# Optimization experiments

Measured on AMD Instinct MI355X. Metric: run time of the kernel, lower is better.

The kernel has to match this reference:

```python
import jax, jax.numpy as jnp
import numpy as np

EPS = 1e-5
NUM_HEADS = 8


def bn(x, gamma, beta, mean, var):
    # eval-mode BatchNorm2d over channel dim (NCHW)
    inv = gamma / jnp.sqrt(var + EPS)
    return x * inv[None, :, None, None] + (beta - mean * inv)[None, :, None, None]


def conv1x1(x, w):
    # w: (O, I, 1, 1) -> pointwise matmul
    return jnp.einsum('bchw,oc->bohw', x, w[:, :, 0, 0])


def conv3x3(x, w):
    return jax.lax.conv_general_dilated(
        x, w, window_strides=(1, 1), padding=((1, 1), (1, 1)),
        dimension_numbers=('NCHW', 'OIHW', 'NCHW'))


def setup_inputs() -> dict:
    key = jax.random.key(0)
    ks = jax.random.split(key, 4)
    B, C, H, W = 2, 256, 64, 64
    return {
        'x': jax.random.normal(ks[0], (B, C, H, W), jnp.float32),
        'w_qkv': jax.random.normal(ks[1], (3 * C, C, 1, 1), jnp.float32) * 0.05,
        'w_local': jax.random.normal(ks[2], (C, C, 3, 3), jnp.float32) * 0.05,
        'local_gamma': jnp.ones((C,), jnp.float32),
        'local_beta': jnp.zeros((C,), jnp.float32),
        'local_mean': jnp.zeros((C,), jnp.float32),
        'local_var': jnp.ones((C,), jnp.float32),
        'w_proj': jax.random.normal(ks[3], (C, C, 1, 1), jnp.float32) * 0.05,
        'proj_gamma': jnp.ones((C,), jnp.float32),
        'proj_beta': jnp.zeros((C,), jnp.float32),
        'proj_mean': jnp.zeros((C,), jnp.float32),
        'proj_var': jnp.ones((C,), jnp.float32),
    }


def reference(x, w_qkv, w_local, local_gamma, local_beta, local_mean, local_var,
              w_proj, proj_gamma, proj_beta, proj_mean, proj_var):
    B, C, H, W = x.shape
    hd = C // NUM_HEADS
    scale = hd ** -0.5
    # qkv: (B, 3C, H, W) -> (B, 3, heads, hd, N)
    qkv = conv1x1(x, w_qkv).reshape(B, 3, NUM_HEADS, hd, H * W)
    q, k, v = qkv[:, 0], qkv[:, 1], qkv[:, 2]  # each (B, heads, hd, N)
    attn = jnp.einsum('bhdn,bhdm->bhnm', q, k) * scale  # (B, heads, N, N)
    attn = jax.nn.softmax(attn, axis=-1)
    out = jnp.einsum('bhnm,bhdm->bhdn', attn, v).reshape(B, C, H, W)
    local_out = bn(conv3x3(x, w_local), local_gamma, local_beta, local_mean, local_var)
    return bn(conv1x1(out + local_out, w_proj), proj_gamma, proj_beta, proj_mean, proj_var)
```

## Files before the change

### kernel.cpp

```cpp
#include <hip/hip_runtime.h>

#define EPSV 1e-5f

typedef unsigned short u16;
typedef unsigned int u32;
typedef __attribute__((ext_vector_type(8))) short bf16x8;
typedef __attribute__((ext_vector_type(4))) float f32x4;

__device__ __forceinline__ u16 f2bf(float f) {
  u32 u = __float_as_uint(f);
  u32 r = (u + 0x7FFFu + ((u >> 16) & 1u)) >> 16;
  return (u16)r;
}
__device__ __forceinline__ float fexp2(float x) {
  float r;
  asm("v_exp_f32 %0, %1" : "=v"(r) : "v"(x));
  return r;
}

#define MFMA(a, b, c) __builtin_amdgcn_mfma_f32_16x16x32_bf16((a), (b), (c), 0, 0, 0)

__global__ __launch_bounds__(256) void prep_kernel(
    const float* __restrict__ x, const float* __restrict__ wqkv,
    const float* __restrict__ wproj, const float* __restrict__ wloc,
    u16* __restrict__ xT, u16* __restrict__ wqkvb,
    u16* __restrict__ wprojb, u16* __restrict__ wb) {
  __shared__ float Ls[16][260];
  const int bid = blockIdx.x;
  const int tid = threadIdx.x;
  if (bid < 512) {
    const int nt = bid & 15, cb = (bid >> 4) & 15, b = bid >> 8;
    const int cc0 = tid >> 6, n4 = (tid & 63) * 4;
    const float* xb = x + ((size_t)(b * 256 + cb * 16)) * 4096 + nt * 256;
#pragma unroll
    for (int j = 0; j < 4; j++) {
      int cc = j * 4 + cc0;
      *(float4*)&Ls[cc][n4] = *(const float4*)(xb + (size_t)cc * 4096 + n4);
    }
    __syncthreads();
    const int n = tid;
    u16 buf[16];
#pragma unroll
    for (int c = 0; c < 16; c++) buf[c] = f2bf(Ls[c][n]);
    u16* dst = xT + ((size_t)cb * 8192 + b * 4096 + nt * 256 + n) * 16;
    *(uint4*)(dst) = *(uint4*)&buf[0];
    *(uint4*)(dst + 8) = *(uint4*)&buf[8];
  } else {
    const int r = bid - 512, c = tid;
    const float QSCALE = 0.17677669529663687f * 1.4426950408889634f;
    if (r < 768) {
      float sc = (r < 256) ? QSCALE : 1.0f;
      wqkvb[r * 256 + c] = f2bf(wqkv[r * 256 + c] * sc);
    } else if (r < 1024) {
      int o = r - 768;
      wprojb[o * 256 + c] = f2bf(wproj[o * 256 + c]);
    } else {
      int o = r - 1024;
      const float* src = wloc + ((size_t)o * 256 + c) * 9;
#pragma unroll
      for (int tap = 0; tap < 9; tap++)
        wb[tap * 65536 + o * 256 + c] = f2bf(src[tap]);
    }
  }
}

__global__ __launch_bounds__(256, 4) void qkvconv_kernel(
    const u16* __restrict__ xT, const u16* __restrict__ wqkvb,
    const u16* __restrict__ wb,
    const float* __restrict__ g, const float* __restrict__ be,
    const float* __restrict__ mu, const float* __restrict__ var,
    u16* __restrict__ Qg, u16* __restrict__ Kg, u16* __restrict__ Vtg,
    u16* __restrict__ localT) {
  const int bid = blockIdx.x;
  const int tid = threadIdx.x, lane = tid & 63, wv = tid >> 6;
  const int n16 = lane & 15, G = lane >> 4;
  if (bid < 768) {
    const int nB = (bid & 63) * 128;
    const int oB = (bid >> 6) * 64;
    const int waveO = oB + (wv >> 1) * 32;
    const int waveN = nB + (wv & 1) * 64;
    f32x4 acc[2][4] = {};
    const u16* Ap = wqkvb + (size_t)(waveO + n16) * 256 + G * 8;
    const u16* Bp = xT + ((size_t)(G >> 1) * 8192 + waveN + n16) * 16 + (G & 1) * 8;
    for (int c0 = 0; c0 < 256; c0 += 32) {
      bf16x8 a0 = *(const bf16x8*)(Ap + c0);
      bf16x8 a1 = *(const bf16x8*)(Ap + 16 * 256 + c0);
      const u16* bp = Bp + (size_t)(c0 >> 4) * 131072;
      bf16x8 b0 = *(const bf16x8*)(bp);
      bf16x8 b1 = *(const bf16x8*)(bp + 256);
      bf16x8 b2 = *(const bf16x8*)(bp + 512);
      bf16x8 b3 = *(const bf16x8*)(bp + 768);
      acc[0][0] = MFMA(a0, b0, acc[0][0]);
      acc[0][1] = MFMA(a0, b1, acc[0][1]);
      acc[0][2] = MFMA(a0, b2, acc[0][2]);
      acc[0][3] = MFMA(a0, b3, acc[0][3]);
      acc[1][0] = MFMA(a1, b0, acc[1][0]);
      acc[1][1] = MFMA(a1, b1, acc[1][1]);
      acc[1][2] = MFMA(a1, b2, acc[1][2]);
      acc[1][3] = MFMA(a1, b3, acc[1][3]);
    }
    const int which = oB >> 8;
    if (which < 2) {
      u16* base = which ? Kg : Qg;
#pragma unroll
      for (int i = 0; i < 2; i++) {
        int o0 = waveO + i * 16 + G * 4;
        int h = (o0 >> 5) & 7, d0 = o0 & 31;
#pragma unroll
        for (int j = 0; j < 4; j++) {
          int s = waveN + j * 16 + n16;
          int b = s >> 12, n = s & 4095;
          u16 pk[4];
#pragma unroll
          for (int r = 0; r < 4; r++) pk[r] = f2bf(acc[i][j][r]);
          *(uint2*)(base + ((size_t)(b * 8 + h) * 4096 + n) * 32 + d0) = *(uint2*)pk;
        }
      }
    } else {
#pragma unroll
      for (int i = 0; i < 2; i++) {
        int o0 = waveO + i * 16 + G * 4;
        int h = (o0 >> 5) & 7, d0 = o0 & 31;
#pragma unroll
        for (int j = 0; j < 4; j++) {
          int s = waveN + j * 16 + n16;
          int b = s >> 12, n = s & 4095;
          u16* vp = Vtg + ((size_t)(b * 8 + h) * 32 + d0) * 4096 + n;
#pragma unroll
          for (int r = 0; r < 4; r++) vp[(size_t)r * 4096] = f2bf(acc[i][j][r]);
        }
      }
    }
  } else {
    const int r0 = bid - 768;
    const int nB = (r0 & 127) * 64;
    const int oB = (r0 >> 7) * 64;
    const int waveO = oB + (wv >> 1) * 32;
    const int waveN = nB + (wv & 1) * 32;
    const int y = (nB >> 6) & 63;
    const int x0 = waveN & 63;
    f32x4 acc[2][2] = {};
    const u16* Ap = wb + (size_t)(waveO + n16) * 256 + G * 8;
    const u16* Bp = xT + ((size_t)(G >> 1) * 8192 + waveN + n16) * 16 + (G & 1) * 8;
    const bf16x8 z = {0, 0, 0, 0, 0, 0, 0, 0};
    for (int c0 = 0; c0 < 256; c0 += 32) {
      const u16* bp = Bp + (size_t)(c0 >> 4) * 131072;
      const u16* ap = Ap + c0;
#pragma unroll
      for (int tap = 0; tap < 9; tap++) {
        const int dy = tap / 3 - 1, dx = tap % 3 - 1;
        int yy = y + dy;
        if ((unsigned)yy >= 64u) continue;
        bf16x8 a0 = *(const bf16x8*)(ap + (size_t)tap * 65536);
        bf16x8 a1 = *(const bf16x8*)(ap + (size_t)tap * 65536 + 16 * 256);
        const int off = dy * 64 + dx;
        bf16x8 b0, b1;
        if (dx == 0) {
          b0 = *(const bf16x8*)(bp + (ptrdiff_t)off * 16);
          b1 = *(const bf16x8*)(bp + (ptrdiff_t)(off + 16) * 16);
        } else {
          bool v0 = (unsigned)(x0 + n16 + dx) < 64u;
          bool v1 = (unsigned)(x0 + 16 + n16 + dx) < 64u;
          int o0 = v0 ? off : 0;
          int o1 = v1 ? (off + 16) : 16;
          bf16x8 t0 = *(const bf16x8*)(bp + (ptrdiff_t)o0 * 16);
          bf16x8 t1 = *(const bf16x8*)(bp + (ptrdiff_t)o1 * 16);
          b0 = v0 ? t0 : z;
          b1 = v1 ? t1 : z;
        }
        acc[0][0] = MFMA(a0, b0, acc[0][0]);
        acc[0][1] = MFMA(a0, b1, acc[0][1]);
        acc[1][0] = MFMA(a1, b0, acc[1][0]);
        acc[1][1] = MFMA(a1, b1, acc[1][1]);
      }
    }
#pragma unroll
    for (int i = 0; i < 2; i++) {
      int o0 = waveO + i * 16 + G * 4;
      float inv[4], sh[4];
#pragma unroll
      for (int r = 0; r < 4; r++) {
        int o = o0 + r;
        float iv = g[o] * rsqrtf(var[o] + EPSV);
        inv[r] = iv; sh[r] = be[o] - mu[o] * iv;
      }
#pragma unroll
      for (int j = 0; j < 2; j++) {
        int s = waveN + j * 16 + n16;
        u16 pk[4];
#pragma unroll
        for (int r = 0; r < 4; r++) pk[r] = f2bf(acc[i][j][r] * inv[r] + sh[r]);
        *(uint2*)(localT + ((size_t)(o0 >> 4) * 8192 + s) * 16 + (o0 & 15)) = *(uint2*)pk;
      }
    }
  }
}

__global__ __launch_bounds__(256, 4) void flash_mfma_kernel(
    const u16* __restrict__ Qg, const u16* __restrict__ Kg,
    const u16* __restrict__ Vtg, u16* __restrict__ attnT) {
  __shared__ u32 Ps[4][32 * 36];
  __shared__ float MX[2][64][20];
  const int bid = blockIdx.x;
  const int bh = bid >> 6, qt = bid & 63;
  const int tid = threadIdx.x, lane = tid & 63, w = tid >> 6;
  const int n16 = lane & 15, G = lane >> 4;
  const int g = w >> 1, mh = w & 1;
  const int b = bh >> 3, h = bh & 7;
  const int qbase = qt * 64 + g * 32;

  const u16* Qp = Qg + ((size_t)bh * 4096 + qbase) * 32;
  const bf16x8 qf0 = *(const bf16x8*)(Qp + (size_t)n16 * 32 + G * 8);
  const bf16x8 qf1 = *(const bf16x8*)(Qp + (size_t)(16 + n16) * 32 + G * 8);

  f32x4 O00 = {0.f,0.f,0.f,0.f}, O01 = {0.f,0.f,0.f,0.f};
  f32x4 O10 = {0.f,0.f,0.f,0.f}, O11 = {0.f,0.f,0.f,0.f};
  float m0 = -3.0e38f, m1 = -3.0e38f, l0 = 0.f, l1 = 0.f;

  const u16* Kb = Kg + ((size_t)bh * 4096 + mh * 2048) * 32;
  const u16* Vb = Vtg + (size_t)bh * 32 * 4096 + mh * 2048;
  u32* Pw = Ps[w];

  bf16x8 kf0 = *(const bf16x8*)(Kb + (size_t)n16 * 32 + G * 8);
  bf16x8 kf1 = *(const bf16x8*)(Kb + (size_t)(16 + n16) * 32 + G * 8);
  bf16x8 kf2 = *(const bf16x8*)(Kb + (size_t)(32 + n16) * 32 + G * 8);
  bf16x8 kf3 = *(const bf16x8*)(Kb + (size_t)(48 + n16) * 32 + G * 8);

  for (int it = 0; it < 32; ++it) {
    const f32x4 z = {0.f, 0.f, 0.f, 0.f};
    f32x4 S0[4], S1[4];
    S0[0] = MFMA(kf0, qf0, z); S1[0] = MFMA(kf0, qf1, z);
    S0[1] = MFMA(kf1, qf0, z); S1[1] = MFMA(kf1, qf1, z);
    S0[2] = MFMA(kf2, qf0, z); S1[2] = MFMA(kf2, qf1, z);
    S0[3] = MFMA(kf3, qf0, z); S1[3] = MFMA(kf3, qf1, z);

    {
      const u16* Kn = Kb + (size_t)(((it + 1) & 31) * 64) * 32;
      kf0 = *(const bf16x8*)(Kn + (size_t)n16 * 32 + G * 8);
      kf1 = *(const bf16x8*)(Kn + (size_t)(16 + n16) * 32 + G * 8);
      kf2 = *(const bf16x8*)(Kn + (size_t)(32 + n16) * 32 + G * 8);
      kf3 = *(const bf16x8*)(Kn + (size_t)(48 + n16) * 32 + G * 8);
    }

    float mt0 = fmaxf(fmaxf(S0[0].x, S0[0].y), fmaxf(S0[0].z, S0[0].w));
    float mt1 = fmaxf(fmaxf(S1[0].x, S1[0].y), fmaxf(S1[0].z, S1[0].w));
#pragma unroll
    for (int t = 1; t < 4; t++) {
      mt0 = fmaxf(mt0, fmaxf(fmaxf(S0[t].x, S0[t].y), fmaxf(S0[t].z, S0[t].w)));
      mt1 = fmaxf(mt1, fmaxf(fmaxf(S1[t].x, S1[t].y), fmaxf(S1[t].z, S1[t].w)));
    }
    mt0 = fmaxf(mt0, __shfl_xor(mt0, 16, 64));
    mt0 = fmaxf(mt0, __shfl_xor(mt0, 32, 64));
    mt1 = fmaxf(mt1, __shfl_xor(mt1, 16, 64));
    mt1 = fmaxf(mt1, __shfl_xor(mt1, 32, 64));
    float mn0 = fmaxf(m0, mt0), mn1 = fmaxf(m1, mt1);
    if (__any((mt0 > m0) | (mt1 > m1))) {
      float a0 = fexp2(m0 - mn0);
      float a1 = fexp2(m1 - mn1);
      l0 *= a0; l1 *= a1;
      O00 *= a0; O01 *= a0; O10 *= a1; O11 *= a1;
    }
    m0 = mn0; m1 = mn1;

#pragma unroll
    for (int t = 0; t < 4; t++) {
      float p0 = fexp2(S0[t].x - m0), p1 = fexp2(S0[t].y - m0);
      float p2 = fexp2(S0[t].z - m0), p3 = fexp2(S0[t].w - m0);
      l0 += (p0 + p1) + (p2 + p3);
      uint2 pr;
      pr.x = __builtin_amdgcn_perm(__float_as_uint(p1), __float_as_uint(p0), 0x07060302u);
      pr.y = __builtin_amdgcn_perm(__float_as_uint(p3), __float_as_uint(p2), 0x07060302u);
      *(uint2*)&Pw[n16 * 36 + 8 * t + 2 * G] = pr;
      float q0 = fexp2(S1[t].x - m1), q1 = fexp2(S1[t].y - m1);
      float q2 = fexp2(S1[t].z - m1), q3 = fexp2(S1[t].w - m1);
      l1 += (q0 + q1) + (q2 + q3);
      uint2 qr;
      qr.x = __builtin_amdgcn_perm(__float_as_uint(q1), __float_as_uint(q0), 0x07060302u);
      qr.y = __builtin_amdgcn_perm(__float_as_uint(q3), __float_as_uint(q2), 0x07060302u);
      *(uint2*)&Pw[(16 + n16) * 36 + 8 * t + 2 * G] = qr;
    }

#pragma unroll
    for (int c = 0; c < 2; c++) {
      const u16* Vp = Vb + (size_t)it * 64 + c * 32 + G * 8;
      bf16x8 va0 = *(const bf16x8*)(Vp + (size_t)n16 * 4096);
      bf16x8 va1 = *(const bf16x8*)(Vp + (size_t)(16 + n16) * 4096);
      union { uint4 u; bf16x8 v; } B0, B1;
      B0.u = *(uint4*)&Pw[n16 * 36 + 16 * c + 4 * G];
      B1.u = *(uint4*)&Pw[(16 + n16) * 36 + 16 * c + 4 * G];
      O00 = MFMA(va0, B0.v, O00);
      O01 = MFMA(va1, B0.v, O01);
      O10 = MFMA(va0, B1.v, O10);
      O11 = MFMA(va1, B1.v, O11);
    }
  }

  if (mh == 1) {
    float* dst = &MX[g][lane][0];
    *(f32x4*)(dst + 0)  = O00;
    *(f32x4*)(dst + 4)  = O01;
    *(f32x4*)(dst + 8)  = O10;
    *(f32x4*)(dst + 12) = O11;
    dst[16] = m0; dst[17] = l0; dst[18] = m1; dst[19] = l1;
  }
  __syncthreads();
  if (mh == 0) {
    const float* src = &MX[g][lane][0];
    f32x4 P00 = *(const f32x4*)(src + 0);
    f32x4 P01 = *(const f32x4*)(src + 4);
    f32x4 P10 = *(const f32x4*)(src + 8);
    f32x4 P11 = *(const f32x4*)(src + 12);
    float pm0 = src[16], pl0 = src[17], pm1 = src[18], pl1 = src[19];

    float M0 = fmaxf(m0, pm0);
    float se0 = fexp2(m0 - M0), so0 = fexp2(pm0 - M0);
    float M1 = fmaxf(m1, pm1);
    float se1 = fexp2(m1 - M1), so1 = fexp2(pm1 - M1);
    float ls0 = l0 * se0 + pl0 * so0;
    float ls1 = l1 * se1 + pl1 * so1;
    ls0 += __shfl_xor(ls0, 16, 64);
    ls0 += __shfl_xor(ls0, 32, 64);
    ls1 += __shfl_xor(ls1, 16, 64);
    ls1 += __shfl_xor(ls1, 32, 64);
    const float rl0 = 1.0f / ls0, rl1 = 1.0f / ls1;

    const int s0 = b * 4096 + qbase + n16;
    const int s1 = s0 + 16;
    const int cb0 = h * 2, cb1 = h * 2 + 1;
    u16 pk[4];
#pragma unroll
    for (int r = 0; r < 4; r++) pk[r] = f2bf((O00[r] * se0 + P00[r] * so0) * rl0);
    *(uint2*)(attnT + ((size_t)cb0 * 8192 + s0) * 16 + G * 4) = *(uint2*)pk;
#pragma unroll
    for (int r = 0; r < 4; r++) pk[r] = f2bf((O01[r] * se0 + P01[r] * so0) * rl0);
    *(uint2*)(attnT + ((size_t)cb1 * 8192 + s0) * 16 + G * 4) = *(uint2*)pk;
#pragma unroll
    for (int r = 0; r < 4; r++) pk[r] = f2bf((O10[r] * se1 + P10[r] * so1) * rl1);
    *(uint2*)(attnT + ((size_t)cb0 * 8192 + s1) * 16 + G * 4) = *(uint2*)pk;
#pragma unroll
    for (int r = 0; r < 4; r++) pk[r] = f2bf((O11[r] * se1 + P11[r] * so1) * rl1);
    *(uint2*)(attnT + ((size_t)cb1 * 8192 + s1) * 16 + G * 4) = *(uint2*)pk;
  }
}

__global__ __launch_bounds__(256, 4) void proj_mfma_kernel(
    const u16* __restrict__ attnT, const u16* __restrict__ localT,
    const u16* __restrict__ wprojb,
    const float* __restrict__ g, const float* __restrict__ be,
    const float* __restrict__ mu, const float* __restrict__ var,
    float* __restrict__ out) {
  const int nB = blockIdx.x * 64;
  const int oB = blockIdx.y * 64;
  const int tid = threadIdx.x, lane = tid & 63, wv = tid >> 6;
  const int n16 = lane & 15, G = lane >> 4;
  const int waveO = oB + (wv >> 1) * 32;
  const int waveN = nB + (wv & 1) * 32;
  f32x4 acc[2][2] = {};
  const u16* Ap = wprojb + (size_t)(waveO + n16) * 256 + G * 8;
  const size_t boff = ((size_t)(G >> 1) * 8192 + waveN + n16) * 16 + (G & 1) * 8;
  for (int c0 = 0; c0 < 256; c0 += 32) {
    bf16x8 a0 = *(const bf16x8*)(Ap + c0);
    bf16x8 a1 = *(const bf16x8*)(Ap + 16 * 256 + c0);
    const size_t bo = boff + (size_t)(c0 >> 4) * 131072;
    bf16x8 p0 = *(const bf16x8*)(attnT + bo);
    bf16x8 p1 = *(const bf16x8*)(attnT + bo + 256);
    bf16x8 q0 = *(const bf16x8*)(localT + bo);
    bf16x8 q1 = *(const bf16x8*)(localT + bo + 256);
    acc[0][0] = MFMA(a0, p0, acc[0][0]);
    acc[0][1] = MFMA(a0, p1, acc[0][1]);
    acc[1][0] = MFMA(a1, p0, acc[1][0]);
    acc[1][1] = MFMA(a1, p1, acc[1][1]);
    acc[0][0] = MFMA(a0, q0, acc[0][0]);
    acc[0][1] = MFMA(a0, q1, acc[0][1]);
    acc[1][0] = MFMA(a1, q0, acc[1][0]);
    acc[1][1] = MFMA(a1, q1, acc[1][1]);
  }
#pragma unroll
  for (int i = 0; i < 2; i++) {
    int o0 = waveO + i * 16 + G * 4;
    float inv[4], sh[4];
#pragma unroll
    for (int r = 0; r < 4; r++) {
      int o = o0 + r;
      float iv = g[o] * rsqrtf(var[o] + EPSV);
      inv[r] = iv; sh[r] = be[o] - mu[o] * iv;
    }
#pragma unroll
    for (int j = 0; j < 2; j++) {
      int s = waveN + j * 16 + n16;
      int b = s >> 12, n = s & 4095;
      float* op = out + ((size_t)(b * 256 + o0)) * 4096 + n;
#pragma unroll
      for (int r = 0; r < 4; r++) op[(size_t)r * 4096] = acc[i][j][r] * inv[r] + sh[r];
    }
  }
}

extern "C" void kernel_launch(void* const* d_in, const int* in_sizes, int n_in,
                              void* d_out, int out_size, void* d_ws, size_t ws_size,
                              hipStream_t stream) {
  (void)in_sizes; (void)n_in; (void)out_size; (void)ws_size;
  const float* x       = (const float*)d_in[0];
  const float* w_qkv   = (const float*)d_in[1];
  const float* w_local = (const float*)d_in[2];
  const float* lg = (const float*)d_in[3];
  const float* lb = (const float*)d_in[4];
  const float* lm = (const float*)d_in[5];
  const float* lv = (const float*)d_in[6];
  const float* w_proj  = (const float*)d_in[7];
  const float* pg = (const float*)d_in[8];
  const float* pb = (const float*)d_in[9];
  const float* pm = (const float*)d_in[10];
  const float* pvr = (const float*)d_in[11];
  float* out = (float*)d_out;

  u16* Q      = (u16*)d_ws;
  u16* K      = Q + 2097152;
  u16* Vt     = K + 2097152;
  u16* xT     = Vt + 2097152;
  u16* attnT  = xT + 2097152;
  u16* localT = attnT + 2097152;
  u16* wqkvb  = localT + 2097152;
  u16* wprojb = wqkvb + 196608;
  u16* wb     = wprojb + 65536;

  hipLaunchKernelGGL(prep_kernel, dim3(1792), dim3(256), 0, stream,
                     x, w_qkv, w_proj, w_local, xT, wqkvb, wprojb, wb);
  hipLaunchKernelGGL(qkvconv_kernel, dim3(1280), dim3(256), 0, stream,
                     xT, wqkvb, wb, lg, lb, lm, lv, Q, K, Vt, localT);
  hipLaunchKernelGGL(flash_mfma_kernel, dim3(1024), dim3(256), 0, stream,
                     Q, K, Vt, attnT);
  hipLaunchKernelGGL(proj_mfma_kernel, dim3(128, 4), dim3(256), 0, stream,
                     attnT, localT, wprojb, pg, pb, pm, pvr, out);
}
```

Before: 236.2 us.

## Shrink tiles, split flash KV across four waves, compute row sums via MFMA

Halves per-block work in the QKV GEMM, 3x3 conv and projection kernels, doubling grid sizes and raising launch-bound occupancy hints. The flash attention kernel now gives each block 32 queries and splits the keys four ways across waves, with a 4-way log-sum-exp merge through shared memory. Row sums of P are accumulated with an MFMA against a ones vector instead of scalar adds. The aim is more parallelism and latency hiding on the GPU's many CUs, at the cost of less register-level reuse, more redundant A/B loads and a heavier final merge.

```diff
diff --git a/kernel.cpp b/kernel.cpp
--- a/kernel.cpp
+++ b/kernel.cpp
@@ -64,7 +64,7 @@
   }
 }
 
-__global__ __launch_bounds__(256, 4) void qkvconv_kernel(
+__global__ __launch_bounds__(256, 6) void qkvconv_kernel(
     const u16* __restrict__ xT, const u16* __restrict__ wqkvb,
     const u16* __restrict__ wb,
     const float* __restrict__ g, const float* __restrict__ be,
@@ -74,12 +74,12 @@
   const int bid = blockIdx.x;
   const int tid = threadIdx.x, lane = tid & 63, wv = tid >> 6;
   const int n16 = lane & 15, G = lane >> 4;
-  if (bid < 768) {
-    const int nB = (bid & 63) * 128;
-    const int oB = (bid >> 6) * 64;
+  if (bid < 1536) {
+    const int oB = (bid >> 7) * 64;
+    const int nB = (bid & 127) * 64;
     const int waveO = oB + (wv >> 1) * 32;
-    const int waveN = nB + (wv & 1) * 64;
-    f32x4 acc[2][4] = {};
+    const int waveN = nB + (wv & 1) * 32;
+    f32x4 acc[2][2] = {};
     const u16* Ap = wqkvb + (size_t)(waveO + n16) * 256 + G * 8;
     const u16* Bp = xT + ((size_t)(G >> 1) * 8192 + waveN + n16) * 16 + (G & 1) * 8;
     for (int c0 = 0; c0 < 256; c0 += 32) {
@@ -88,16 +88,10 @@
       const u16* bp = Bp + (size_t)(c0 >> 4) * 131072;
       bf16x8 b0 = *(const bf16x8*)(bp);
       bf16x8 b1 = *(const bf16x8*)(bp + 256);
-      bf16x8 b2 = *(const bf16x8*)(bp + 512);
-      bf16x8 b3 = *(const bf16x8*)(bp + 768);
       acc[0][0] = MFMA(a0, b0, acc[0][0]);
       acc[0][1] = MFMA(a0, b1, acc[0][1]);
-      acc[0][2] = MFMA(a0, b2, acc[0][2]);
-      acc[0][3] = MFMA(a0, b3, acc[0][3]);
       acc[1][0] = MFMA(a1, b0, acc[1][0]);
       acc[1][1] = MFMA(a1, b1, acc[1][1]);
-      acc[1][2] = MFMA(a1, b2, acc[1][2]);
-      acc[1][3] = MFMA(a1, b3, acc[1][3]);
     }
     const int which = oB >> 8;
     if (which < 2) {
@@ -107,7 +101,7 @@
         int o0 = waveO + i * 16 + G * 4;
         int h = (o0 >> 5) & 7, d0 = o0 & 31;
 #pragma unroll
-        for (int j = 0; j < 4; j++) {
+        for (int j = 0; j < 2; j++) {
           int s = waveN + j * 16 + n16;
           int b = s >> 12, n = s & 4095;
           u16 pk[4];
@@ -122,7 +116,7 @@
         int o0 = waveO + i * 16 + G * 4;
         int h = (o0 >> 5) & 7, d0 = o0 & 31;
 #pragma unroll
-        for (int j = 0; j < 4; j++) {
+        for (int j = 0; j < 2; j++) {
           int s = waveN + j * 16 + n16;
           int b = s >> 12, n = s & 4095;
           u16* vp = Vtg + ((size_t)(b * 8 + h) * 32 + d0) * 4096 + n;
@@ -132,14 +126,14 @@
       }
     }
   } else {
-    const int r0 = bid - 768;
-    const int nB = (r0 & 127) * 64;
-    const int oB = (r0 >> 7) * 64;
+    const int r0 = bid - 1536;
+    const int oB = (r0 >> 8) * 64;
+    const int nB = (r0 & 255) * 32;
     const int waveO = oB + (wv >> 1) * 32;
-    const int waveN = nB + (wv & 1) * 32;
-    const int y = (nB >> 6) & 63;
+    const int waveN = nB + (wv & 1) * 16;
+    const int y = (waveN >> 6) & 63;
     const int x0 = waveN & 63;
-    f32x4 acc[2][2] = {};
+    f32x4 acc[2] = {};
     const u16* Ap = wb + (size_t)(waveO + n16) * 256 + G * 8;
     const u16* Bp = xT + ((size_t)(G >> 1) * 8192 + waveN + n16) * 16 + (G & 1) * 8;
     const bf16x8 z = {0, 0, 0, 0, 0, 0, 0, 0};
@@ -154,24 +148,17 @@
         bf16x8 a0 = *(const bf16x8*)(ap + (size_t)tap * 65536);
         bf16x8 a1 = *(const bf16x8*)(ap + (size_t)tap * 65536 + 16 * 256);
         const int off = dy * 64 + dx;
-        bf16x8 b0, b1;
+        bf16x8 b0;
         if (dx == 0) {
           b0 = *(const bf16x8*)(bp + (ptrdiff_t)off * 16);
-          b1 = *(const bf16x8*)(bp + (ptrdiff_t)(off + 16) * 16);
         } else {
           bool v0 = (unsigned)(x0 + n16 + dx) < 64u;
-          bool v1 = (unsigned)(x0 + 16 + n16 + dx) < 64u;
           int o0 = v0 ? off : 0;
-          int o1 = v1 ? (off + 16) : 16;
           bf16x8 t0 = *(const bf16x8*)(bp + (ptrdiff_t)o0 * 16);
-          bf16x8 t1 = *(const bf16x8*)(bp + (ptrdiff_t)o1 * 16);
           b0 = v0 ? t0 : z;
-          b1 = v1 ? t1 : z;
         }
-        acc[0][0] = MFMA(a0, b0, acc[0][0]);
-        acc[0][1] = MFMA(a0, b1, acc[0][1]);
-        acc[1][0] = MFMA(a1, b0, acc[1][0]);
-        acc[1][1] = MFMA(a1, b1, acc[1][1]);
+        acc[0] = MFMA(a0, b0, acc[0]);
+        acc[1] = MFMA(a1, b0, acc[1]);
       }
     }
 #pragma unroll
@@ -184,49 +171,53 @@
         float iv = g[o] * rsqrtf(var[o] + EPSV);
         inv[r] = iv; sh[r] = be[o] - mu[o] * iv;
       }
-#pragma unroll
-      for (int j = 0; j < 2; j++) {
-        int s = waveN + j * 16 + n16;
-        u16 pk[4];
-#pragma unroll
-        for (int r = 0; r < 4; r++) pk[r] = f2bf(acc[i][j][r] * inv[r] + sh[r]);
-        *(uint2*)(localT + ((size_t)(o0 >> 4) * 8192 + s) * 16 + (o0 & 15)) = *(uint2*)pk;
-      }
-    }
-  }
-}
-
-__global__ __launch_bounds__(256, 4) void flash_mfma_kernel(
+      int s = waveN + n16;
+      u16 pk[4];
+#pragma unroll
+      for (int r = 0; r < 4; r++) pk[r] = f2bf(acc[i][r] * inv[r] + sh[r]);
+      *(uint2*)(localT + ((size_t)(o0 >> 4) * 8192 + s) * 16 + (o0 & 15)) = *(uint2*)pk;
+    }
+  }
+}
+
+__global__ __launch_bounds__(256, 7) void flash_mfma_kernel(
     const u16* __restrict__ Qg, const u16* __restrict__ Kg,
     const u16* __restrict__ Vtg, u16* __restrict__ attnT) {
-  __shared__ u32 Ps[4][32 * 36];
-  __shared__ float MX[2][64][20];
+  __shared__ u32 SMEM[4608];
   const int bid = blockIdx.x;
-  const int bh = bid >> 6, qt = bid & 63;
+  const int bh = bid >> 7, qt = bid & 127;
   const int tid = threadIdx.x, lane = tid & 63, w = tid >> 6;
   const int n16 = lane & 15, G = lane >> 4;
-  const int g = w >> 1, mh = w & 1;
   const int b = bh >> 3, h = bh & 7;
-  const int qbase = qt * 64 + g * 32;
+  const int qbase = qt * 32;
 
   const u16* Qp = Qg + ((size_t)bh * 4096 + qbase) * 32;
   const bf16x8 qf0 = *(const bf16x8*)(Qp + (size_t)n16 * 32 + G * 8);
   const bf16x8 qf1 = *(const bf16x8*)(Qp + (size_t)(16 + n16) * 32 + G * 8);
 
+  bf16x8 onesA;
+  {
+    union { bf16x8 v; u16 u[8]; } o1;
+#pragma unroll
+    for (int i = 0; i < 8; i++) o1.u[i] = 0x3F80;
+    onesA = o1.v;
+  }
+
   f32x4 O00 = {0.f,0.f,0.f,0.f}, O01 = {0.f,0.f,0.f,0.f};
   f32x4 O10 = {0.f,0.f,0.f,0.f}, O11 = {0.f,0.f,0.f,0.f};
-  float m0 = -3.0e38f, m1 = -3.0e38f, l0 = 0.f, l1 = 0.f;
-
-  const u16* Kb = Kg + ((size_t)bh * 4096 + mh * 2048) * 32;
-  const u16* Vb = Vtg + (size_t)bh * 32 * 4096 + mh * 2048;
-  u32* Pw = Ps[w];
+  f32x4 L0 = {0.f,0.f,0.f,0.f}, L1 = {0.f,0.f,0.f,0.f};
+  float m0 = -3.0e38f, m1 = -3.0e38f;
+
+  const u16* Kb = Kg + ((size_t)bh * 4096 + w * 1024) * 32;
+  const u16* Vb = Vtg + (size_t)bh * 32 * 4096 + w * 1024;
+  u32* Pw = SMEM + w * 1152;
 
   bf16x8 kf0 = *(const bf16x8*)(Kb + (size_t)n16 * 32 + G * 8);
   bf16x8 kf1 = *(const bf16x8*)(Kb + (size_t)(16 + n16) * 32 + G * 8);
   bf16x8 kf2 = *(const bf16x8*)(Kb + (size_t)(32 + n16) * 32 + G * 8);
   bf16x8 kf3 = *(const bf16x8*)(Kb + (size_t)(48 + n16) * 32 + G * 8);
 
-  for (int it = 0; it < 32; ++it) {
+  for (int it = 0; it < 16; ++it) {
     const f32x4 z = {0.f, 0.f, 0.f, 0.f};
     f32x4 S0[4], S1[4];
     S0[0] = MFMA(kf0, qf0, z); S1[0] = MFMA(kf0, qf1, z);
@@ -235,7 +226,7 @@
     S0[3] = MFMA(kf3, qf0, z); S1[3] = MFMA(kf3, qf1, z);
 
     {
-      const u16* Kn = Kb + (size_t)(((it + 1) & 31) * 64) * 32;
+      const u16* Kn = Kb + (size_t)(((it + 1) & 15) * 64) * 32;
       kf0 = *(const bf16x8*)(Kn + (size_t)n16 * 32 + G * 8);
       kf1 = *(const bf16x8*)(Kn + (size_t)(16 + n16) * 32 + G * 8);
       kf2 = *(const bf16x8*)(Kn + (size_t)(32 + n16) * 32 + G * 8);
@@ -257,7 +248,7 @@
     if (__any((mt0 > m0) | (mt1 > m1))) {
       float a0 = fexp2(m0 - mn0);
       float a1 = fexp2(m1 - mn1);
-      l0 *= a0; l1 *= a1;
+      L0 *= a0; L1 *= a1;
       O00 *= a0; O01 *= a0; O10 *= a1; O11 *= a1;
     }
     m0 = mn0; m1 = mn1;
@@ -266,14 +257,12 @@
     for (int t = 0; t < 4; t++) {
       float p0 = fexp2(S0[t].x - m0), p1 = fexp2(S0[t].y - m0);
       float p2 = fexp2(S0[t].z - m0), p3 = fexp2(S0[t].w - m0);
-      l0 += (p0 + p1) + (p2 + p3);
       uint2 pr;
       pr.x = __builtin_amdgcn_perm(__float_as_uint(p1), __float_as_uint(p0), 0x07060302u);
       pr.y = __builtin_amdgcn_perm(__float_as_uint(p3), __float_as_uint(p2), 0x07060302u);
       *(uint2*)&Pw[n16 * 36 + 8 * t + 2 * G] = pr;
       float q0 = fexp2(S1[t].x - m1), q1 = fexp2(S1[t].y - m1);
       float q2 = fexp2(S1[t].z - m1), q3 = fexp2(S1[t].w - m1);
-      l1 += (q0 + q1) + (q2 + q3);
       uint2 qr;
       qr.x = __builtin_amdgcn_perm(__float_as_uint(q1), __float_as_uint(q0), 0x07060302u);
       qr.y = __builtin_amdgcn_perm(__float_as_uint(q3), __float_as_uint(q2), 0x07060302u);
@@ -290,109 +279,108 @@
       B1.u = *(uint4*)&Pw[(16 + n16) * 36 + 16 * c + 4 * G];
       O00 = MFMA(va0, B0.v, O00);
       O01 = MFMA(va1, B0.v, O01);
+      L0  = MFMA(onesA, B0.v, L0);
       O10 = MFMA(va0, B1.v, O10);
       O11 = MFMA(va1, B1.v, O11);
-    }
-  }
-
-  if (mh == 1) {
-    float* dst = &MX[g][lane][0];
+      L1  = MFMA(onesA, B1.v, L1);
+    }
+  }
+
+  __syncthreads();
+  float* MXf = (float*)SMEM;
+  if (w > 0) {
+    float* dst = MXf + ((size_t)(w - 1) * 64 + lane) * 20;
     *(f32x4*)(dst + 0)  = O00;
     *(f32x4*)(dst + 4)  = O01;
     *(f32x4*)(dst + 8)  = O10;
     *(f32x4*)(dst + 12) = O11;
-    dst[16] = m0; dst[17] = l0; dst[18] = m1; dst[19] = l1;
+    dst[16] = m0; dst[17] = L0.x; dst[18] = m1; dst[19] = L1.x;
   }
   __syncthreads();
-  if (mh == 0) {
-    const float* src = &MX[g][lane][0];
-    f32x4 P00 = *(const f32x4*)(src + 0);
-    f32x4 P01 = *(const f32x4*)(src + 4);
-    f32x4 P10 = *(const f32x4*)(src + 8);
-    f32x4 P11 = *(const f32x4*)(src + 12);
-    float pm0 = src[16], pl0 = src[17], pm1 = src[18], pl1 = src[19];
-
-    float M0 = fmaxf(m0, pm0);
-    float se0 = fexp2(m0 - M0), so0 = fexp2(pm0 - M0);
-    float M1 = fmaxf(m1, pm1);
-    float se1 = fexp2(m1 - M1), so1 = fexp2(pm1 - M1);
-    float ls0 = l0 * se0 + pl0 * so0;
-    float ls1 = l1 * se1 + pl1 * so1;
-    ls0 += __shfl_xor(ls0, 16, 64);
-    ls0 += __shfl_xor(ls0, 32, 64);
-    ls1 += __shfl_xor(ls1, 16, 64);
-    ls1 += __shfl_xor(ls1, 32, 64);
-    const float rl0 = 1.0f / ls0, rl1 = 1.0f / ls1;
-
-    const int s0 = b * 4096 + qbase + n16;
-    const int s1 = s0 + 16;
+  if (w == 0) {
+    float M0 = m0, M1 = m1;
+#pragma unroll
+    for (int ww = 0; ww < 3; ww++) {
+      const float* src = MXf + ((size_t)ww * 64 + lane) * 20;
+      M0 = fmaxf(M0, src[16]);
+      M1 = fmaxf(M1, src[18]);
+    }
+    float se0 = fexp2(m0 - M0), se1 = fexp2(m1 - M1);
+    f32x4 A00 = O00 * se0, A01 = O01 * se0;
+    f32x4 A10 = O10 * se1, A11 = O11 * se1;
+    float l0 = L0.x * se0, l1 = L1.x * se1;
+#pragma unroll
+    for (int ww = 0; ww < 3; ww++) {
+      const float* src = MXf + ((size_t)ww * 64 + lane) * 20;
+      float s0 = fexp2(src[16] - M0), s1 = fexp2(src[18] - M1);
+      A00 += *(const f32x4*)(src + 0) * s0;
+      A01 += *(const f32x4*)(src + 4) * s0;
+      A10 += *(const f32x4*)(src + 8) * s1;
+      A11 += *(const f32x4*)(src + 12) * s1;
+      l0 += src[17] * s0;
+      l1 += src[19] * s1;
+    }
+    const float rl0 = 1.0f / l0, rl1 = 1.0f / l1;
+    const int s0i = b * 4096 + qbase + n16;
+    const int s1i = s0i + 16;
     const int cb0 = h * 2, cb1 = h * 2 + 1;
     u16 pk[4];
 #pragma unroll
-    for (int r = 0; r < 4; r++) pk[r] = f2bf((O00[r] * se0 + P00[r] * so0) * rl0);
-    *(uint2*)(attnT + ((size_t)cb0 * 8192 + s0) * 16 + G * 4) = *(uint2*)pk;
-#pragma unroll
-    for (int r = 0; r < 4; r++) pk[r] = f2bf((O01[r] * se0 + P01[r] * so0) * rl0);
-    *(uint2*)(attnT + ((size_t)cb1 * 8192 + s0) * 16 + G * 4) = *(uint2*)pk;
-#pragma unroll
-    for (int r = 0; r < 4; r++) pk[r] = f2bf((O10[r] * se1 + P10[r] * so1) * rl1);
-    *(uint2*)(attnT + ((size_t)cb0 * 8192 + s1) * 16 + G * 4) = *(uint2*)pk;
-#pragma unroll
-    for (int r = 0; r < 4; r++) pk[r] = f2bf((O11[r] * se1 + P11[r] * so1) * rl1);
-    *(uint2*)(attnT + ((size_t)cb1 * 8192 + s1) * 16 + G * 4) = *(uint2*)pk;
-  }
-}
-
-__global__ __launch_bounds__(256, 4) void proj_mfma_kernel(
+    for (int r = 0; r < 4; r++) pk[r] = f2bf(A00[r] * rl0);
+    *(uint2*)(attnT + ((size_t)cb0 * 8192 + s0i) * 16 + G * 4) = *(uint2*)pk;
+#pragma unroll
+    for (int r = 0; r < 4; r++) pk[r] = f2bf(A01[r] * rl0);
+    *(uint2*)(attnT + ((size_t)cb1 * 8192 + s0i) * 16 + G * 4) = *(uint2*)pk;
+#pragma unroll
+    for (int r = 0; r < 4; r++) pk[r] = f2bf(A10[r] * rl1);
+    *(uint2*)(attnT + ((size_t)cb0 * 8192 + s1i) * 16 + G * 4) = *(uint2*)pk;
+#pragma unroll
+    for (int r = 0; r < 4; r++) pk[r] = f2bf(A11[r] * rl1);
+    *(uint2*)(attnT + ((size_t)cb1 * 8192 + s1i) * 16 + G * 4) = *(uint2*)pk;
+  }
+}
+
+__global__ __launch_bounds__(256, 6) void proj_mfma_kernel(
     const u16* __restrict__ attnT, const u16* __restrict__ localT,
     const u16* __restrict__ wprojb,
     const float* __restrict__ g, const float* __restrict__ be,
     const float* __restrict__ mu, const float* __restrict__ var,
     float* __restrict__ out) {
-  const int nB = blockIdx.x * 64;
+  const int nB = blockIdx.x * 32;
   const int oB = blockIdx.y * 64;
   const int tid = threadIdx.x, lane = tid & 63, wv = tid >> 6;
   const int n16 = lane & 15, G = lane >> 4;
-  const int waveO = oB + (wv >> 1) * 32;
-  const int waveN = nB + (wv & 1) * 32;
-  f32x4 acc[2][2] = {};
+  const int waveO = oB + wv * 16;
+  f32x4 acc[2] = {};
   const u16* Ap = wprojb + (size_t)(waveO + n16) * 256 + G * 8;
-  const size_t boff = ((size_t)(G >> 1) * 8192 + waveN + n16) * 16 + (G & 1) * 8;
+  const size_t boff = ((size_t)(G >> 1) * 8192 + nB + n16) * 16 + (G & 1) * 8;
   for (int c0 = 0; c0 < 256; c0 += 32) {
     bf16x8 a0 = *(const bf16x8*)(Ap + c0);
-    bf16x8 a1 = *(const bf16x8*)(Ap + 16 * 256 + c0);
     const size_t bo = boff + (size_t)(c0 >> 4) * 131072;
     bf16x8 p0 = *(const bf16x8*)(attnT + bo);
     bf16x8 p1 = *(const bf16x8*)(attnT + bo + 256);
     bf16x8 q0 = *(const bf16x8*)(localT + bo);
     bf16x8 q1 = *(const bf16x8*)(localT + bo + 256);
-    acc[0][0] = MFMA(a0, p0, acc[0][0]);
-    acc[0][1] = MFMA(a0, p1, acc[0][1]);
-    acc[1][0] = MFMA(a1, p0, acc[1][0]);
-    acc[1][1] = MFMA(a1, p1, acc[1][1]);
-    acc[0][0] = MFMA(a0, q0, acc[0][0]);
-    acc[0][1] = MFMA(a0, q1, acc[0][1]);
-    acc[1][0] = MFMA(a1, q0, acc[1][0]);
-    acc[1][1] = MFMA(a1, q1, acc[1][1]);
-  }
-#pragma unroll
-  for (int i = 0; i < 2; i++) {
-    int o0 = waveO + i * 16 + G * 4;
-    float inv[4], sh[4];
-#pragma unroll
-    for (int r = 0; r < 4; r++) {
-      int o = o0 + r;
-      float iv = g[o] * rsqrtf(var[o] + EPSV);
-      inv[r] = iv; sh[r] = be[o] - mu[o] * iv;
-    }
-#pragma unroll
-    for (int j = 0; j < 2; j++) {
-      int s = waveN + j * 16 + n16;
-      int b = s >> 12, n = s & 4095;
-      float* op = out + ((size_t)(b * 256 + o0)) * 4096 + n;
-#pragma unroll
-      for (int r = 0; r < 4; r++) op[(size_t)r * 4096] = acc[i][j][r] * inv[r] + sh[r];
-    }
+    acc[0] = MFMA(a0, p0, acc[0]);
+    acc[1] = MFMA(a0, p1, acc[1]);
+    acc[0] = MFMA(a0, q0, acc[0]);
+    acc[1] = MFMA(a0, q1, acc[1]);
+  }
+  int o0 = waveO + G * 4;
+  float inv[4], sh[4];
+#pragma unroll
+  for (int r = 0; r < 4; r++) {
+    int o = o0 + r;
+    float iv = g[o] * rsqrtf(var[o] + EPSV);
+    inv[r] = iv; sh[r] = be[o] - mu[o] * iv;
+  }
+#pragma unroll
+  for (int j = 0; j < 2; j++) {
+    int s = nB + j * 16 + n16;
+    int b = s >> 12, n = s & 4095;
+    float* op = out + ((size_t)(b * 256 + o0)) * 4096 + n;
+#pragma unroll
+    for (int r = 0; r < 4; r++) op[(size_t)r * 4096] = acc[j][r] * inv[r] + sh[r];
   }
 }
 
@@ -426,10 +414,10 @@
 
   hipLaunchKernelGGL(prep_kernel, dim3(1792), dim3(256), 0, stream,
                      x, w_qkv, w_proj, w_local, xT, wqkvb, wprojb, wb);
-  hipLaunchKernelGGL(qkvconv_kernel, dim3(1280), dim3(256), 0, stream,
+  hipLaunchKernelGGL(qkvconv_kernel, dim3(2560), dim3(256), 0, stream,
                      xT, wqkvb, wb, lg, lb, lm, lv, Q, K, Vt, localT);
-  hipLaunchKernelGGL(flash_mfma_kernel, dim3(1024), dim3(256), 0, stream,
+  hipLaunchKernelGGL(flash_mfma_kernel, dim3(2048), dim3(256), 0, stream,
                      Q, K, Vt, attnT);
-  hipLaunchKernelGGL(proj_mfma_kernel, dim3(128, 4), dim3(256), 0, stream,
+  hipLaunchKernelGGL(proj_mfma_kernel, dim3(256, 4), dim3(256), 0, stream,
                      attnT, localT, wprojb, pg, pb, pm, pvr, out);
 }
```

Result: slower. 517.9 us (+119.3%).

## Move 3x3 conv blocks from QKV kernel into flash attention kernel launch

Applied to the files above, without the earlier changes.

Splits the QKV projection into its own kernel and merges the 3x3 local conv work into the flash attention launch. Blocks are interleaved so that every third block runs a conv tile and the rest run attention tiles. The conv, which is independent of attention, can then overlap with the attention work and fill idle CUs instead of lengthening the QKV stage. The cost is that conv blocks now carry the attention kernel's shared-memory footprint and register pressure, and attention tiles are spread across more blocks.

```diff
diff --git a/kernel.cpp b/kernel.cpp
--- a/kernel.cpp
+++ b/kernel.cpp
@@ -64,77 +64,89 @@
   }
 }
 
-__global__ __launch_bounds__(256, 4) void qkvconv_kernel(
+__global__ __launch_bounds__(256, 4) void qkv_kernel(
     const u16* __restrict__ xT, const u16* __restrict__ wqkvb,
-    const u16* __restrict__ wb,
-    const float* __restrict__ g, const float* __restrict__ be,
-    const float* __restrict__ mu, const float* __restrict__ var,
-    u16* __restrict__ Qg, u16* __restrict__ Kg, u16* __restrict__ Vtg,
-    u16* __restrict__ localT) {
+    u16* __restrict__ Qg, u16* __restrict__ Kg, u16* __restrict__ Vtg) {
   const int bid = blockIdx.x;
   const int tid = threadIdx.x, lane = tid & 63, wv = tid >> 6;
   const int n16 = lane & 15, G = lane >> 4;
-  if (bid < 768) {
-    const int nB = (bid & 63) * 128;
-    const int oB = (bid >> 6) * 64;
-    const int waveO = oB + (wv >> 1) * 32;
-    const int waveN = nB + (wv & 1) * 64;
-    f32x4 acc[2][4] = {};
-    const u16* Ap = wqkvb + (size_t)(waveO + n16) * 256 + G * 8;
-    const u16* Bp = xT + ((size_t)(G >> 1) * 8192 + waveN + n16) * 16 + (G & 1) * 8;
-    for (int c0 = 0; c0 < 256; c0 += 32) {
-      bf16x8 a0 = *(const bf16x8*)(Ap + c0);
-      bf16x8 a1 = *(const bf16x8*)(Ap + 16 * 256 + c0);
-      const u16* bp = Bp + (size_t)(c0 >> 4) * 131072;
-      bf16x8 b0 = *(const bf16x8*)(bp);
-      bf16x8 b1 = *(const bf16x8*)(bp + 256);
-      bf16x8 b2 = *(const bf16x8*)(bp + 512);
-      bf16x8 b3 = *(const bf16x8*)(bp + 768);
-      acc[0][0] = MFMA(a0, b0, acc[0][0]);
-      acc[0][1] = MFMA(a0, b1, acc[0][1]);
-      acc[0][2] = MFMA(a0, b2, acc[0][2]);
-      acc[0][3] = MFMA(a0, b3, acc[0][3]);
-      acc[1][0] = MFMA(a1, b0, acc[1][0]);
-      acc[1][1] = MFMA(a1, b1, acc[1][1]);
-      acc[1][2] = MFMA(a1, b2, acc[1][2]);
-      acc[1][3] = MFMA(a1, b3, acc[1][3]);
-    }
-    const int which = oB >> 8;
-    if (which < 2) {
-      u16* base = which ? Kg : Qg;
-#pragma unroll
-      for (int i = 0; i < 2; i++) {
-        int o0 = waveO + i * 16 + G * 4;
-        int h = (o0 >> 5) & 7, d0 = o0 & 31;
-#pragma unroll
-        for (int j = 0; j < 4; j++) {
-          int s = waveN + j * 16 + n16;
-          int b = s >> 12, n = s & 4095;
-          u16 pk[4];
-#pragma unroll
-          for (int r = 0; r < 4; r++) pk[r] = f2bf(acc[i][j][r]);
-          *(uint2*)(base + ((size_t)(b * 8 + h) * 4096 + n) * 32 + d0) = *(uint2*)pk;
-        }
+  const int nB = (bid & 63) * 128;
+  const int oB = (bid >> 6) * 64;
+  const int waveO = oB + (wv >> 1) * 32;
+  const int waveN = nB + (wv & 1) * 64;
+  f32x4 acc[2][4] = {};
+  const u16* Ap = wqkvb + (size_t)(waveO + n16) * 256 + G * 8;
+  const u16* Bp = xT + ((size_t)(G >> 1) * 8192 + waveN + n16) * 16 + (G & 1) * 8;
+  for (int c0 = 0; c0 < 256; c0 += 32) {
+    bf16x8 a0 = *(const bf16x8*)(Ap + c0);
+    bf16x8 a1 = *(const bf16x8*)(Ap + 16 * 256 + c0);
+    const u16* bp = Bp + (size_t)(c0 >> 4) * 131072;
+    bf16x8 b0 = *(const bf16x8*)(bp);
+    bf16x8 b1 = *(const bf16x8*)(bp + 256);
+    bf16x8 b2 = *(const bf16x8*)(bp + 512);
+    bf16x8 b3 = *(const bf16x8*)(bp + 768);
+    acc[0][0] = MFMA(a0, b0, acc[0][0]);
+    acc[0][1] = MFMA(a0, b1, acc[0][1]);
+    acc[0][2] = MFMA(a0, b2, acc[0][2]);
+    acc[0][3] = MFMA(a0, b3, acc[0][3]);
+    acc[1][0] = MFMA(a1, b0, acc[1][0]);
+    acc[1][1] = MFMA(a1, b1, acc[1][1]);
+    acc[1][2] = MFMA(a1, b2, acc[1][2]);
+    acc[1][3] = MFMA(a1, b3, acc[1][3]);
+  }
+  const int which = oB >> 8;
+  if (which < 2) {
+    u16* base = which ? Kg : Qg;
+#pragma unroll
+    for (int i = 0; i < 2; i++) {
+      int o0 = waveO + i * 16 + G * 4;
+      int h = (o0 >> 5) & 7, d0 = o0 & 31;
+#pragma unroll
+      for (int j = 0; j < 4; j++) {
+        int s = waveN + j * 16 + n16;
+        int b = s >> 12, n = s & 4095;
+        u16 pk[4];
+#pragma unroll
+        for (int r = 0; r < 4; r++) pk[r] = f2bf(acc[i][j][r]);
+        *(uint2*)(base + ((size_t)(b * 8 + h) * 4096 + n) * 32 + d0) = *(uint2*)pk;
       }
-    } else {
-#pragma unroll
-      for (int i = 0; i < 2; i++) {
-        int o0 = waveO + i * 16 + G * 4;
-        int h = (o0 >> 5) & 7, d0 = o0 & 31;
-#pragma unroll
-        for (int j = 0; j < 4; j++) {
-          int s = waveN + j * 16 + n16;
-          int b = s >> 12, n = s & 4095;
-          u16* vp = Vtg + ((size_t)(b * 8 + h) * 32 + d0) * 4096 + n;
-#pragma unroll
-          for (int r = 0; r < 4; r++) vp[(size_t)r * 4096] = f2bf(acc[i][j][r]);
-        }
+    }
+  } else {
+#pragma unroll
+    for (int i = 0; i < 2; i++) {
+      int o0 = waveO + i * 16 + G * 4;
+      int h = (o0 >> 5) & 7, d0 = o0 & 31;
+#pragma unroll
+      for (int j = 0; j < 4; j++) {
+        int s = waveN + j * 16 + n16;
+        int b = s >> 12, n = s & 4095;
+        u16* vp = Vtg + ((size_t)(b * 8 + h) * 32 + d0) * 4096 + n;
+#pragma unroll
+        for (int r = 0; r < 4; r++) vp[(size_t)r * 4096] = f2bf(acc[i][j][r]);
       }
     }
-  } else {
-    const int r0 = bid - 768;
-    const int nB = (r0 & 127) * 64;
-    const int oB = (r0 >> 7) * 64;
+  }
+}
+
+__global__ __launch_bounds__(256, 4) void flashconv_kernel(
+    const u16* __restrict__ Qg, const u16* __restrict__ Kg,
+    const u16* __restrict__ Vtg, u16* __restrict__ attnT,
+    const u16* __restrict__ xT, const u16* __restrict__ wb,
+    const float* __restrict__ g, const float* __restrict__ be,
+    const float* __restrict__ mu, const float* __restrict__ var,
+    u16* __restrict__ localT) {
+  __shared__ u32 Ps[4][32 * 36];
+  __shared__ float MX[2][64][20];
+  const int bid = blockIdx.x;
+  const int tid = threadIdx.x, lane = tid & 63;
+  const int n16 = lane & 15, G = lane >> 4;
+  const int sel = bid % 3;
+
+  if (sel == 2) {
+    const int cidx = bid / 3;
+    const int wv = tid >> 6;
+    const int nB = (cidx & 127) * 64;
+    const int oB = (cidx >> 7) * 64;
     const int waveO = oB + (wv >> 1) * 32;
     const int waveN = nB + (wv & 1) * 32;
     const int y = (nB >> 6) & 63;
@@ -193,21 +205,15 @@
         *(uint2*)(localT + ((size_t)(o0 >> 4) * 8192 + s) * 16 + (o0 & 15)) = *(uint2*)pk;
       }
     }
-  }
-}
-
-__global__ __launch_bounds__(256, 4) void flash_mfma_kernel(
-    const u16* __restrict__ Qg, const u16* __restrict__ Kg,
-    const u16* __restrict__ Vtg, u16* __restrict__ attnT) {
-  __shared__ u32 Ps[4][32 * 36];
-  __shared__ float MX[2][64][20];
-  const int bid = blockIdx.x;
-  const int bh = bid >> 6, qt = bid & 63;
-  const int tid = threadIdx.x, lane = tid & 63, w = tid >> 6;
-  const int n16 = lane & 15, G = lane >> 4;
-  const int g = w >> 1, mh = w & 1;
+    return;
+  }
+
+  const int fidx = (bid / 3) * 2 + sel;
+  const int bh = fidx >> 6, qt = fidx & 63;
+  const int w = tid >> 6;
+  const int gq = w >> 1, mh = w & 1;
   const int b = bh >> 3, h = bh & 7;
-  const int qbase = qt * 64 + g * 32;
+  const int qbase = qt * 64 + gq * 32;
 
   const u16* Qp = Qg + ((size_t)bh * 4096 + qbase) * 32;
   const bf16x8 qf0 = *(const bf16x8*)(Qp + (size_t)n16 * 32 + G * 8);
@@ -296,7 +302,7 @@
   }
 
   if (mh == 1) {
-    float* dst = &MX[g][lane][0];
+    float* dst = &MX[gq][lane][0];
     *(f32x4*)(dst + 0)  = O00;
     *(f32x4*)(dst + 4)  = O01;
     *(f32x4*)(dst + 8)  = O10;
@@ -305,7 +311,7 @@
   }
   __syncthreads();
   if (mh == 0) {
-    const float* src = &MX[g][lane][0];
+    const float* src = &MX[gq][lane][0];
     f32x4 P00 = *(const f32x4*)(src + 0);
     f32x4 P01 = *(const f32x4*)(src + 4);
     f32x4 P10 = *(const f32x4*)(src + 8);
@@ -426,10 +432,10 @@
 
   hipLaunchKernelGGL(prep_kernel, dim3(1792), dim3(256), 0, stream,
                      x, w_qkv, w_proj, w_local, xT, wqkvb, wprojb, wb);
-  hipLaunchKernelGGL(qkvconv_kernel, dim3(1280), dim3(256), 0, stream,
-                     xT, wqkvb, wb, lg, lb, lm, lv, Q, K, Vt, localT);
-  hipLaunchKernelGGL(flash_mfma_kernel, dim3(1024), dim3(256), 0, stream,
-                     Q, K, Vt, attnT);
+  hipLaunchKernelGGL(qkv_kernel, dim3(768), dim3(256), 0, stream,
+                     xT, wqkvb, Q, K, Vt);
+  hipLaunchKernelGGL(flashconv_kernel, dim3(1536), dim3(256), 0, stream,
+                     Q, K, Vt, attnT, xT, wb, lg, lb, lm, lv, localT);
   hipLaunchKernelGGL(proj_mfma_kernel, dim3(128, 4), dim3(256), 0, stream,
                      attnT, localT, wprojb, pg, pb, pm, pvr, out);
 }
```

After: 259.8 us. +10.0%, slower.
